# Optimization experiments

Measured on AMD Instinct MI355X. Metric: run time of the kernel, lower is better.

Reference implementation:

```python
import jax, jax.numpy as jnp
import numpy as np

EPS = 1e-5


def _bn_relu(y, g, beta, relu=True):
    # BatchNorm1d in training mode: biased batch stats over (B, V) per channel
    mean = jnp.mean(y, axis=(0, 2), keepdims=True)
    var = jnp.mean((y - mean) ** 2, axis=(0, 2), keepdims=True)
    out = (y - mean) * jax.lax.rsqrt(var + EPS) * g[None, :, None] + beta[None, :, None]
    return jnp.maximum(out, 0.0) if relu else out


def _spiral_conv(x, idx, w, b, g, beta):
    # x: (B,C,V), idx: (V,L) -> gather (B,C,V,L), row-major reshape to (B,C*L,V)
    B, C, V = x.shape
    L = idx.shape[1]
    neigh = x[:, :, idx].reshape(B, C * L, V)
    y = jnp.einsum('om,bmv->bov', w, neigh) + b[None, :, None]
    return _bn_relu(y, g, beta)


def _se(x, w1, w2):
    s = jnp.mean(x, axis=2)                              # (B,C)
    h = jnp.maximum(jnp.einsum('bc,rc->br', s, w1), 0.0)  # (B,r)
    s = jax.nn.sigmoid(jnp.einsum('br,cr->bc', h, w2))   # (B,C)
    return x * s[:, :, None]


def setup_inputs() -> dict:
    key = jax.random.key(0)
    ks = jax.random.split(key, 24)
    B, V, L, H = 2, 16384, 12, 256
    sc = 0.05
    inp = {
        'verts': jax.random.normal(ks[0], (B, V, 3), jnp.float32),
        'spirals': jax.random.randint(ks[1], (4, V, L), 0, V, jnp.int32),
        'enc0_w': jax.random.normal(ks[2], (H, 3 * L), jnp.float32) * sc,
        'enc0_b': jax.random.normal(ks[3], (H,), jnp.float32) * sc,
        'enc0_g': jnp.ones((H,), jnp.float32),
        'enc0_beta': jnp.zeros((H,), jnp.float32),
        'enc_w': jax.random.normal(ks[4], (3, H, H * L), jnp.float32) * sc,
        'enc_b': jax.random.normal(ks[5], (3, H), jnp.float32) * sc,
        'enc_g': jnp.ones((3, H), jnp.float32),
        'enc_beta': jnp.zeros((3, H), jnp.float32),
        'se_w1': jax.random.normal(ks[6], (4, H // 8, H), jnp.float32) * sc,
        'se_w2': jax.random.normal(ks[7], (4, H, H // 8), jnp.float32) * sc,
        'skip_w': jax.random.normal(ks[8], (3, H, 2 * H), jnp.float32) * sc,
        'skip_b': jax.random.normal(ks[9], (3, H), jnp.float32) * sc,
        'dec_w': jax.random.normal(ks[10], (3, H, H * L), jnp.float32) * sc,
        'dec_b': jax.random.normal(ks[11], (3, H), jnp.float32) * sc,
        'dec_g': jnp.ones((3, H), jnp.float32),
        'dec_beta': jnp.zeros((3, H), jnp.float32),
        'cls1_w': jax.random.normal(ks[12], (H // 2, H), jnp.float32) * sc,
        'cls1_b': jax.random.normal(ks[13], (H // 2,), jnp.float32) * sc,
        'cls1_g': jnp.ones((H // 2,), jnp.float32),
        'cls1_beta': jnp.zeros((H // 2,), jnp.float32),
        'cls2_w': jax.random.normal(ks[14], (H // 4, H // 2), jnp.float32) * sc,
        'cls2_b': jax.random.normal(ks[15], (H // 4,), jnp.float32) * sc,
        'cls2_g': jnp.ones((H // 4,), jnp.float32),
        'cls2_beta': jnp.zeros((H // 4,), jnp.float32),
        'cls3_w': jax.random.normal(ks[16], (1, H // 4), jnp.float32) * sc,
        'cls3_b': jax.random.normal(ks[17], (1,), jnp.float32) * sc,
    }
    return inp


def reference(verts, spirals, enc0_w, enc0_b, enc0_g, enc0_beta,
              enc_w, enc_b, enc_g, enc_beta, se_w1, se_w2,
              skip_w, skip_b, dec_w, dec_b, dec_g, dec_beta,
              cls1_w, cls1_b, cls1_g, cls1_beta,
              cls2_w, cls2_b, cls2_g, cls2_beta, cls3_w, cls3_b):
    x = jnp.transpose(verts, (0, 2, 1))  # (B,3,V)
    feats = []
    # encoder: 4 blocks, block0 has no residual (3 != 256)
    for i in range(4):
        if i == 0:
            out = _spiral_conv(x, spirals[0], enc0_w, enc0_b, enc0_g, enc0_beta)
        else:
            out = _spiral_conv(x, spirals[i], enc_w[i - 1], enc_b[i - 1], enc_g[i - 1], enc_beta[i - 1]) + x
        x = _se(out, se_w1[i], se_w2[i])
        feats.append(x)
    # decoder with skip-concat fusion, spirals[2],[1],[0] and feats[2],[1],[0]
    for i in range(3):
        feat = feats[2 - i]
        idx = spirals[2 - i]
        xc = jnp.concatenate([x, feat], axis=1)  # (B,512,V)
        x = jnp.einsum('oc,bcv->bov', skip_w[i], xc) + skip_b[i][None, :, None]
        x = _spiral_conv(x, idx, dec_w[i], dec_b[i], dec_g[i], dec_beta[i]) + x
    # classifier: 1x1 conv stack
    h = _bn_relu(jnp.einsum('oc,bcv->bov', cls1_w, x) + cls1_b[None, :, None], cls1_g, cls1_beta)
    h = _bn_relu(jnp.einsum('oc,bcv->bov', cls2_w, h) + cls2_b[None, :, None], cls2_g, cls2_beta)
    out = jnp.einsum('oc,bcv->bov', cls3_w, h) + cls3_b[None, :, None]  # (B,1,V)
    return out[:, 0, :]  # (B,V)
```

## Files before the change

### kernel.cpp

```cpp
#include <hip/hip_runtime.h>

typedef unsigned short u16;
using f16x8 = __attribute__((ext_vector_type(8))) _Float16;
using f32x4 = __attribute__((ext_vector_type(4))) float;

#define V_N 16384
#define M_N 32768

__device__ __forceinline__ float h2f(u16 u) {
  _Float16 h; __builtin_memcpy(&h, &u, 2); return (float)h;
}
__device__ __forceinline__ u16 f2h(float f) {
  _Float16 h = (_Float16)f; u16 u; __builtin_memcpy(&u, &h, 2); return u;
}

__device__ __forceinline__ void dma16(const u16* g, u16* l) {
  __builtin_amdgcn_global_load_lds(
      (const __attribute__((address_space(1))) void*)(const void*)g,
      (__attribute__((address_space(3))) void*)(void*)l, 16, 0, 0);
}

__global__ __launch_bounds__(256) void perm2_k(const float* __restrict__ w, u16* __restrict__ wp) {
  int o = blockIdx.x & 255, layer = blockIdx.x >> 8;
  int t = threadIdx.x;
  const float* src = w + ((size_t)layer * 256 + o) * 3072;
  u16* dst = wp + (size_t)layer * 786432;
  float2 v[6];
  #pragma unroll
  for (int q = 0; q < 6; ++q) v[q] = *(const float2*)(src + t * 12 + q * 2);
  const float* vf = (const float*)v;
  int lo = t & 31;
  #pragma unroll
  for (int m = 0; m < 12; ++m) {
    int kc = m * 8 + (t >> 5);
    dst[(size_t)kc * 8192 + o * 32 + lo] = f2h(vf[m]);
  }
}

__global__ __launch_bounds__(256) void permfr_k(const float* __restrict__ src, u16* __restrict__ dst,
                                                int O, int K) {
  int i = blockIdx.x * 256 + threadIdx.x;
  if (i >= (K << 8)) return;
  int j = i & 7, lq = (i >> 3) & 3, col = (i >> 5) & 255, kc = i >> 13;
  int k = kc * 32 + lq * 8 + j;
  float v = (col < O) ? src[(size_t)col * K + k] : 0.f;
  dst[i] = f2h(v);
}

__global__ __launch_bounds__(256) void wscale_k(const u16* __restrict__ w, const float* __restrict__ sig,
                                                const float* __restrict__ sigx,
                                                u16* __restrict__ o, int n, int sel) {
  int i = blockIdx.x * 256 + threadIdx.x;
  if (i >= n) return;
  float wv = h2f(w[i]);
  int k = (i >> 13) * 32 + ((i >> 3) & 3) * 8 + (i & 7);
  int c = k & 255;
  #pragma unroll
  for (int b = 0; b < 2; ++b) {
    float s;
    if (sel == 511 && k < 256) s = sigx ? sigx[b * 256 + c] : 1.f;
    else                       s = sig[b * 256 + c];
    o[(long)b * n + i] = f2h(wv * s);
  }
}

__global__ __launch_bounds__(256) void enc0_k(const float* __restrict__ verts, const int* __restrict__ sp,
                                              const float* __restrict__ w0, u16* __restrict__ y) {
  __shared__ float xs[32][36];
  int t = threadIdx.x;
  int r0 = blockIdx.x * 32;
  for (int s = t; s < 32 * 12; s += 256) {
    int row = s / 12, tt = s - row * 12;
    int gr = r0 + row;
    int b = gr >> 14, v = gr & (V_N - 1);
    int j = sp[tt * V_N + v];
    const float* p = verts + ((long)b * V_N + j) * 3;
    xs[row][tt]      = p[0];
    xs[row][12 + tt] = p[1];
    xs[row][24 + tt] = p[2];
  }
  __syncthreads();
  float w[36];
  #pragma unroll
  for (int k = 0; k < 36; ++k) w[k] = w0[t * 36 + k];
  for (int row = 0; row < 32; ++row) {
    float a = 0.f;
    #pragma unroll
    for (int k = 0; k < 36; ++k) a += w[k] * xs[row][k];
    y[(long)(r0 + row) * 256 + t] = f2h(a);
  }
}

template<int CT>
__global__ __launch_bounds__(512, 4) void gemm3_k(
    const u16* __restrict__ P0, const u16* __restrict__ P1, int lda,
    const int* __restrict__ sp, int L,
    const u16* __restrict__ Wt, long wstride,
    u16* __restrict__ Yb, const float* __restrict__ bias, int Ostore,
    float* __restrict__ stats)
{
  constexpr int KC   = CT >> 5;
  constexpr int PH   = (CT == 256) ? 4 : 2;
  constexpr int KCP  = KC / PH;
  constexpr int PROW = 64;
  __shared__ __align__(16) u16 lA[2][64 * PROW];
  const int tid  = threadIdx.x;
  const int wave = tid >> 6, lane = tid & 63;
  const int wn = wave * 32;
  const int lr = lane & 15, lq = lane >> 4;
  const int nwg = gridDim.x;
  const int wg = (blockIdx.x & 7) * (nwg >> 3) + (blockIdx.x >> 3);
  const int bm = wg * 64;
  const int batch = bm >> 14;
  const int vbase = bm & (V_N - 1);
  const int qrow = lane >> 3;
  const int qchunk = lane & 7;
  const bool gat = (sp != nullptr);
  const long rowb = (long)batch * V_N;
  const u16* Pd1 = P1 ? P1 : P0;
  const u16* Wb = Wt + (long)batch * wstride;
  const int NS = PH * L;

  const u16* bp[2];
  #pragma unroll
  for (int nt = 0; nt < 2; ++nt)
    bp[nt] = Wb + ((long)(wn + nt * 16 + lr) * 4 + lq) * 8;

  auto load_idx = [&](int tap) -> int {
    int v = 0;
    if (gat && lane < 8) v = sp[(long)tap * V_N + vbase + wave * 8 + lane];
    return v;
  };

  auto dma_st = [&](int sb, const u16* src, int idxreg, int ph) {
    u16* wb = lA[sb] + wave * (8 * PROW);
    int rloc = wave * 8 + qrow;
    long grow;
    if (gat) grow = rowb + (long)__shfl(idxreg, qrow, 64);
    else     grow = bm + rloc;
    const u16* gp = src + grow * lda + ph * PROW + ((qchunk ^ (rloc & 7)) << 3);
    dma16(gp, wb);
  };

  auto loadB = [&](int cb, f16x8 (&tB)[KCP * 2]) {
    #pragma unroll
    for (int kp = 0; kp < KCP; ++kp)
      #pragma unroll
      for (int nt = 0; nt < 2; ++nt)
        tB[kp * 2 + nt] = *(const f16x8*)(bp[nt] + (long)(cb + kp) * 8192);
  };

  f32x4 acc[4][2];
  #pragma unroll
  for (int i = 0; i < 4; ++i)
    #pragma unroll
    for (int j = 0; j < 2; ++j) acc[i][j] = (f32x4){0.f, 0.f, 0.f, 0.f};

  auto compute_st = [&](int sb, const f16x8 (&tB)[KCP * 2]) {
    #pragma unroll
    for (int kp = 0; kp < KCP; ++kp) {
      f16x8 a[4];
      #pragma unroll
      for (int mt = 0; mt < 4; ++mt) {
        int row = mt * 16 + lr;
        a[mt] = *(const f16x8*)(&lA[sb][row * PROW + (((kp * 4 + lq) ^ (row & 7)) << 3)]);
      }
      #pragma unroll
      for (int mt = 0; mt < 4; ++mt)
        #pragma unroll
        for (int nt = 0; nt < 2; ++nt)
          acc[mt][nt] = __builtin_amdgcn_mfma_f32_16x16x32_f16(a[mt], tB[kp * 2 + nt], acc[mt][nt], 0, 0, 0);
    }
  };

  f16x8 tBc[KCP * 2], tBn[KCP * 2];

  int idxC = load_idx(0);
  dma_st(0, P0, idxC, 0);
  loadB(0, tBc);
  int idxN = (gat && L > 1) ? load_idx(1) : idxC;

  int l = 0, ph = 0;
  for (int s = 0; s < NS; ++s) {
    int ln  = (l + 1 == L) ? 0 : l + 1;
    int phn = (l + 1 == L) ? ph + 1 : ph;
    __syncthreads();
    if (s + 1 < NS) {
      const u16* srcN = (!gat && ln > 0) ? Pd1 : P0;
      dma_st((s + 1) & 1, srcN, idxN, phn);
      loadB(ln * KC + phn * KCP, tBn);
    }
    int idxF = 0;
    if (gat && s + 2 < NS) {
      int l2 = (ln + 1 == L) ? 0 : ln + 1;
      idxF = load_idx(l2);
    }
    compute_st(s & 1, tBc);
    #pragma unroll
    for (int i = 0; i < KCP * 2; ++i) tBc[i] = tBn[i];
    idxN = idxF;
    l = ln; ph = phn;
  }

  #pragma unroll
  for (int nt = 0; nt < 2; ++nt) {
    int col = wn + nt * 16 + lr;
    if (col < Ostore) {
      float bv = bias ? bias[col] : 0.f;
      float s1 = 0.f, s2 = 0.f;
      #pragma unroll
      for (int mt = 0; mt < 4; ++mt) {
        #pragma unroll
        for (int rg = 0; rg < 4; ++rg) {
          int row = bm + mt * 16 + lq * 4 + rg;
          float v = acc[mt][nt][rg] + bv;
          Yb[(long)row * Ostore + col] = f2h(v);
          s1 += v; s2 += v * v;
        }
      }
      if (stats) {
        s1 += __shfl_xor(s1, 16); s1 += __shfl_xor(s1, 32);
        s2 += __shfl_xor(s2, 16); s2 += __shfl_xor(s2, 32);
        if (lq == 0) {
          atomicAdd(&stats[col], s1);
          atomicAdd(&stats[Ostore + col], s2);
        }
      }
    }
  }
}

__global__ __launch_bounds__(256) void stats2_k(const u16* __restrict__ y, float* __restrict__ st) {
  __shared__ float s1L[256], s2L[256];
  int tid = threadIdx.x;
  int ci = (tid & 63) * 4;
  int r0 = blockIdx.x * 64 + (tid >> 6);
  float a1[4] = {0,0,0,0}, a2[4] = {0,0,0,0};
  for (int it = 0; it < 16; ++it) {
    long i = ((long)r0 + it * 4) * 256 + ci;
    uint2 pv = *(const uint2*)(y + i);
    float v0 = h2f((u16)(pv.x & 0xffff)), v1 = h2f((u16)(pv.x >> 16));
    float v2 = h2f((u16)(pv.y & 0xffff)), v3 = h2f((u16)(pv.y >> 16));
    a1[0] += v0; a1[1] += v1; a1[2] += v2; a1[3] += v3;
    a2[0] += v0*v0; a2[1] += v1*v1; a2[2] += v2*v2; a2[3] += v3*v3;
  }
  s1L[tid] = 0.f; s2L[tid] = 0.f;
  __syncthreads();
  #pragma unroll
  for (int j = 0; j < 4; ++j) { atomicAdd(&s1L[ci + j], a1[j]); atomicAdd(&s2L[ci + j], a2[j]); }
  __syncthreads();
  atomicAdd(&st[tid], s1L[tid]);
  atomicAdd(&st[256 + tid], s2L[tid]);
}

__global__ __launch_bounds__(256) void bnrelu2_k(
    const u16* __restrict__ y, const float* __restrict__ st,
    const float* __restrict__ g, const float* __restrict__ be,
    const u16* __restrict__ resid, const float* __restrict__ rscale,
    u16* __restrict__ ob, float* __restrict__ ses, int O)
{
  __shared__ float sL[256];
  int tid = threadIdx.x;
  int tpr = O >> 2;
  int rpi = 256 / tpr;
  int ci = (tid & (tpr - 1)) * 4;
  int row0 = blockIdx.x * (rpi * 16);
  int r0 = row0 + (tid / tpr);
  int b = row0 >> 14;
  float mean[4], sc[4], sh[4], rs[4];
  #pragma unroll
  for (int j = 0; j < 4; ++j) {
    int c = ci + j;
    float m = st[c] * (1.f / 32768.f);
    float var = st[O + c] * (1.f / 32768.f) - m * m;
    mean[j] = m;
    sc[j] = rsqrtf(fmaxf(var, 0.f) + 1e-5f) * g[c];
    sh[j] = be[c];
    rs[j] = rscale ? rscale[b * 256 + c] : 1.f;
  }
  float ss[4] = {0,0,0,0};
  for (int it = 0; it < 16; ++it) {
    long i = ((long)r0 + (long)it * rpi) * O + ci;
    uint2 pv = *(const uint2*)(y + i);
    float v[4];
    v[0] = fmaxf((h2f((u16)(pv.x & 0xffff)) - mean[0]) * sc[0] + sh[0], 0.f);
    v[1] = fmaxf((h2f((u16)(pv.x >> 16))    - mean[1]) * sc[1] + sh[1], 0.f);
    v[2] = fmaxf((h2f((u16)(pv.y & 0xffff)) - mean[2]) * sc[2] + sh[2], 0.f);
    v[3] = fmaxf((h2f((u16)(pv.y >> 16))    - mean[3]) * sc[3] + sh[3], 0.f);
    if (resid) {
      uint2 rv = *(const uint2*)(resid + i);
      v[0] += h2f((u16)(rv.x & 0xffff)) * rs[0]; v[1] += h2f((u16)(rv.x >> 16)) * rs[1];
      v[2] += h2f((u16)(rv.y & 0xffff)) * rs[2]; v[3] += h2f((u16)(rv.y >> 16)) * rs[3];
    }
    uint2 pk;
    pk.x = (unsigned)f2h(v[0]) | ((unsigned)f2h(v[1]) << 16);
    pk.y = (unsigned)f2h(v[2]) | ((unsigned)f2h(v[3]) << 16);
    *(uint2*)(ob + i) = pk;
    #pragma unroll
    for (int j = 0; j < 4; ++j) ss[j] += v[j];
  }
  if (ses) {
    sL[tid] = 0.f;
    __syncthreads();
    #pragma unroll
    for (int j = 0; j < 4; ++j) atomicAdd(&sL[ci + j], ss[j]);
    __syncthreads();
    atomicAdd(&ses[b * O + tid], sL[tid]);
  }
}

__global__ void se_k(const float* __restrict__ ses, const float* __restrict__ w1,
                     const float* __restrict__ w2, float* __restrict__ sig)
{
  __shared__ float s[256];
  __shared__ float h[32];
  int b = blockIdx.x, t = threadIdx.x;
  s[t] = ses[b * 256 + t] * (1.f / 16384.f);
  __syncthreads();
  if (t < 32) {
    float a = 0.f;
    for (int c = 0; c < 256; ++c) a += w1[t * 256 + c] * s[c];
    h[t] = fmaxf(a, 0.f);
  }
  __syncthreads();
  float a = 0.f;
  #pragma unroll
  for (int r = 0; r < 32; ++r) a += w2[t * 32 + r] * h[r];
  sig[b * 256 + t] = 1.f / (1.f + expf(-a));
}

__global__ __launch_bounds__(256) void cls3_k(const u16* __restrict__ h2, const float* __restrict__ w,
                                              const float* __restrict__ b, float* __restrict__ out)
{
  __shared__ float ws[64];
  int t = threadIdx.x;
  if (t < 64) ws[t] = w[t];
  __syncthreads();
  int r = blockIdx.x * 256 + t;
  const u16* p = h2 + (long)r * 64;
  float a = b[0];
  #pragma unroll
  for (int c = 0; c < 64; ++c) a += ws[c] * h2f(p[c]);
  out[r] = a;
}

extern "C" void kernel_launch(void* const* d_in, const int* in_sizes, int n_in,
                              void* d_out, int out_size, void* d_ws, size_t ws_size,
                              hipStream_t stream)
{
  (void)in_sizes; (void)n_in; (void)out_size; (void)ws_size;
  const float* verts   = (const float*)d_in[0];
  const int*   spirals = (const int*)d_in[1];
  const float* enc0_w  = (const float*)d_in[2];
  const float* enc0_g  = (const float*)d_in[4];
  const float* enc0_be = (const float*)d_in[5];
  const float* enc_w   = (const float*)d_in[6];
  const float* enc_g   = (const float*)d_in[8];
  const float* enc_be  = (const float*)d_in[9];
  const float* se_w1   = (const float*)d_in[10];
  const float* se_w2   = (const float*)d_in[11];
  const float* skip_w  = (const float*)d_in[12];
  const float* skip_b  = (const float*)d_in[13];
  const float* dec_w   = (const float*)d_in[14];
  const float* dec_g   = (const float*)d_in[16];
  const float* dec_be  = (const float*)d_in[17];
  const float* cls1_w  = (const float*)d_in[18];
  const float* cls1_g  = (const float*)d_in[20];
  const float* cls1_be = (const float*)d_in[21];
  const float* cls2_w  = (const float*)d_in[22];
  const float* cls2_g  = (const float*)d_in[24];
  const float* cls2_be = (const float*)d_in[25];
  const float* cls3_w  = (const float*)d_in[26];
  const float* cls3_b  = (const float*)d_in[27];

  char* p = (char*)d_ws;
  auto alloc = [&](size_t n) { char* q = p; p += (n + 255) & ~(size_t)255; return q; };
  u16* wpe     = (u16*)alloc((size_t)6 * 256 * 3072 * 2);
  u16* wpe_s   = (u16*)alloc((size_t)3 * 2 * 256 * 3072 * 2);
  u16* skip_wb = (u16*)alloc((size_t)3 * 256 * 512 * 2);
  u16* skip_s  = (u16*)alloc((size_t)3 * 2 * 256 * 512 * 2);
  u16* cls1_wb = (u16*)alloc((size_t)256 * 256 * 2);
  u16* wp6     = (u16*)alloc((size_t)256 * 128 * 2);
  float* stats = (float*)alloc(2048);
  float* sesum = (float*)alloc(2048);
  float* sig   = (float*)alloc(4 * 2048);
  u16* out0 = (u16*)alloc((size_t)M_N * 256 * 2);
  u16* out1 = (u16*)alloc((size_t)M_N * 256 * 2);
  u16* out2 = (u16*)alloc((size_t)M_N * 256 * 2);
  u16* ct   = (u16*)alloc((size_t)M_N * 256 * 2);
  u16* tb   = (u16*)alloc((size_t)M_N * 256 * 2);
  u16* xd   = (u16*)alloc((size_t)M_N * 256 * 2);
  u16* outs[4] = {out0, out1, out2, ct};
  const size_t WENC = (size_t)256 * 3072;
  const size_t WSKP = (size_t)256 * 512;

  perm2_k<<<768, 256, 0, stream>>>(enc_w, wpe);
  perm2_k<<<768, 256, 0, stream>>>(dec_w, wpe + (size_t)3 * WENC);
  for (int s = 0; s < 3; ++s)
    permfr_k<<<512, 256, 0, stream>>>(skip_w + (size_t)s * 256 * 512,
                                      skip_wb + (size_t)s * WSKP, 256, 512);
  permfr_k<<<256, 256, 0, stream>>>(cls1_w, cls1_wb, 128, 256);
  permfr_k<<<128, 256, 0, stream>>>(cls2_w, wp6, 64, 128);

  hipMemsetAsync(stats, 0, 4096, stream);
  enc0_k<<<1024, 256, 0, stream>>>(verts, spirals, enc0_w, ct);
  stats2_k<<<512, 256, 0, stream>>>(ct, stats);
  bnrelu2_k<<<512, 256, 0, stream>>>(ct, stats, enc0_g, enc0_be, nullptr, nullptr, out0, sesum, 256);
  se_k<<<2, 256, 0, stream>>>(sesum, se_w1, se_w2, sig);

  for (int i = 1; i < 4; ++i) {
    wscale_k<<<3072, 256, 0, stream>>>(wpe + (size_t)(i - 1) * WENC, sig + (i - 1) * 512, nullptr,
                                       wpe_s + (size_t)(i - 1) * 2 * WENC, (int)WENC, 255);
    hipMemsetAsync(stats, 0, 4096, stream);
    gemm3_k<256><<<512, 512, 0, stream>>>(outs[i - 1], nullptr, 256,
                                          spirals + (size_t)i * V_N * 12, 12,
                                          wpe_s + (size_t)(i - 1) * 2 * WENC, (long)WENC,
                                          ct, nullptr, 256, stats);
    bnrelu2_k<<<512, 256, 0, stream>>>(ct, stats, enc_g + (i - 1) * 256, enc_be + (i - 1) * 256,
                                       outs[i - 1], sig + (i - 1) * 512, outs[i], sesum, 256);
    se_k<<<2, 256, 0, stream>>>(sesum, se_w1 + (size_t)i * 32 * 256,
                                se_w2 + (size_t)i * 256 * 32, sig + i * 512);
  }

  for (int i = 0; i < 3; ++i) {
    wscale_k<<<512, 256, 0, stream>>>(skip_wb + (size_t)i * WSKP, sig + (2 - i) * 512,
                                      (i == 0) ? (sig + 3 * 512) : nullptr,
                                      skip_s + (size_t)i * 2 * WSKP, (int)WSKP, 511);
    gemm3_k<256><<<512, 512, 0, stream>>>((i == 0) ? ct : xd, outs[2 - i], 256, nullptr, 2,
                                          skip_s + (size_t)i * 2 * WSKP, (long)WSKP,
                                          tb, skip_b + i * 256, 256, nullptr);
    hipMemsetAsync(stats, 0, 4096, stream);
    gemm3_k<256><<<512, 512, 0, stream>>>(tb, nullptr, 256,
                                          spirals + (size_t)(2 - i) * V_N * 12, 12,
                                          wpe + (size_t)(3 + i) * WENC, 0,
                                          outs[2 - i], nullptr, 256, stats);
    bnrelu2_k<<<512, 256, 0, stream>>>(outs[2 - i], stats, dec_g + i * 256, dec_be + i * 256,
                                       tb, nullptr, xd, nullptr, 256);
  }

  hipMemsetAsync(stats, 0, 4096, stream);
  gemm3_k<256><<<512, 512, 0, stream>>>(xd, nullptr, 256, nullptr, 1,
                                        cls1_wb, 0, ct, nullptr, 128, stats);
  bnrelu2_k<<<256, 256, 0, stream>>>(ct, stats, cls1_g, cls1_be, nullptr, nullptr, ct, nullptr, 128);
  hipMemsetAsync(stats, 0, 4096, stream);
  gemm3_k<128><<<512, 512, 0, stream>>>(ct, nullptr, 128, nullptr, 1,
                                        wp6, 0, tb, nullptr, 64, stats);
  bnrelu2_k<<<128, 256, 0, stream>>>(tb, stats, cls2_g, cls2_be, nullptr, nullptr, tb, nullptr, 64);
  cls3_k<<<128, 256, 0, stream>>>(tb, cls3_w, cls3_b, (float*)d_out);
}
```

Baseline: 914.3 us.

## Triple-buffer gathered A tiles in LDS with prefetch distance two

Replaces the double-buffered LDS pipeline in the spiral gather GEMM with a three-buffer ring. The gather DMA for stage s+2 is issued while stage s computes, and manual s_waitcnt/s_barrier with sched_barriers replace __syncthreads. The loop is unrolled by two so the B-register ping-pong works without copying tBn into tBc. The aim is to hide more of the irregular gather latency. In exchange it uses more LDS, which can lower occupancy, and the hard-coded vmcnt values depend on an exact per-thread count of outstanding loads, which is fragile across template instantiations.

```diff
diff --git a/kernel.cpp b/kernel.cpp
--- a/kernel.cpp
+++ b/kernel.cpp
@@ -103,7 +103,8 @@
   constexpr int PH   = (CT == 256) ? 4 : 2;
   constexpr int KCP  = KC / PH;
   constexpr int PROW = 64;
-  __shared__ __align__(16) u16 lA[2][64 * PROW];
+  constexpr int BUFE = 64 * PROW;
+  __shared__ __align__(16) u16 lA[3 * BUFE];
   const int tid  = threadIdx.x;
   const int wave = tid >> 6, lane = tid & 63;
   const int wn = wave * 32;
@@ -132,8 +133,8 @@
     return v;
   };
 
-  auto dma_st = [&](int sb, const u16* src, int idxreg, int ph) {
-    u16* wb = lA[sb] + wave * (8 * PROW);
+  auto dma_st = [&](u16* buf, const u16* src, int idxreg, int ph) {
+    u16* wb = buf + wave * (8 * PROW);
     int rloc = wave * 8 + qrow;
     long grow;
     if (gat) grow = rowb + (long)__shfl(idxreg, qrow, 64);
@@ -156,14 +157,14 @@
     #pragma unroll
     for (int j = 0; j < 2; ++j) acc[i][j] = (f32x4){0.f, 0.f, 0.f, 0.f};
 
-  auto compute_st = [&](int sb, const f16x8 (&tB)[KCP * 2]) {
+  auto compute_st = [&](const u16* buf, const f16x8 (&tB)[KCP * 2]) {
     #pragma unroll
     for (int kp = 0; kp < KCP; ++kp) {
       f16x8 a[4];
       #pragma unroll
       for (int mt = 0; mt < 4; ++mt) {
         int row = mt * 16 + lr;
-        a[mt] = *(const f16x8*)(&lA[sb][row * PROW + (((kp * 4 + lq) ^ (row & 7)) << 3)]);
+        a[mt] = *(const f16x8*)(&buf[row * PROW + (((kp * 4 + lq) ^ (row & 7)) << 3)]);
       }
       #pragma unroll
       for (int mt = 0; mt < 4; ++mt)
@@ -173,33 +174,51 @@
     }
   };
 
-  f16x8 tBc[KCP * 2], tBn[KCP * 2];
-
-  int idxC = load_idx(0);
-  dma_st(0, P0, idxC, 0);
-  loadB(0, tBc);
-  int idxN = (gat && L > 1) ? load_idx(1) : idxC;
-
-  int l = 0, ph = 0;
-  for (int s = 0; s < NS; ++s) {
-    int ln  = (l + 1 == L) ? 0 : l + 1;
-    int phn = (l + 1 == L) ? ph + 1 : ph;
-    __syncthreads();
-    if (s + 1 < NS) {
-      const u16* srcN = (!gat && ln > 0) ? Pd1 : P0;
-      dma_st((s + 1) & 1, srcN, idxN, phn);
-      loadB(ln * KC + phn * KCP, tBn);
+  f16x8 tA[KCP * 2], tB2[KCP * 2];
+
+  auto adv = [&](int& l, int& ph) { if (++l == L) { l = 0; ++ph; } };
+  int lB = 0, phB = 0; adv(lB, phB);
+  int lD = lB, phD = phB; adv(lD, phD);
+  int lI = lD; { int pT = phD; int lT = lI; adv(lT, pT); lI = lT; }
+  int idxN;
+
+  {
+    int i0 = load_idx(0);
+    int i1 = load_idx(lB);
+    idxN = load_idx(lD);
+    dma_st(lA, P0, i0, 0);
+    if (NS > 1) {
+      const u16* s1 = (!gat && lB > 0) ? Pd1 : P0;
+      dma_st(lA + BUFE, s1, i1, phB);
     }
-    int idxF = 0;
-    if (gat && s + 2 < NS) {
-      int l2 = (ln + 1 == L) ? 0 : ln + 1;
-      idxF = load_idx(l2);
+    __builtin_amdgcn_sched_barrier(0);
+    loadB(0, tA);
+    __builtin_amdgcn_sched_barrier(0);
+  }
+
+  auto stage = [&](int s, f16x8 (&tCur)[KCP * 2], f16x8 (&tNxt)[KCP * 2]) {
+    if (s + 1 < NS) asm volatile("s_waitcnt vmcnt(5)" ::: "memory");
+    else            asm volatile("s_waitcnt vmcnt(0)" ::: "memory");
+    asm volatile("s_waitcnt lgkmcnt(0)" ::: "memory");
+    __builtin_amdgcn_s_barrier();
+    __builtin_amdgcn_sched_barrier(0);
+    if (s + 1 < NS) loadB(lB * KC + phB * KCP, tNxt);
+    __builtin_amdgcn_sched_barrier(0);
+    int idxT = 0;
+    if (gat && s + 3 < NS) idxT = load_idx(lI);
+    if (s + 2 < NS) {
+      const u16* srcD = (!gat && lD > 0) ? Pd1 : P0;
+      dma_st(lA + ((s + 2) % 3) * BUFE, srcD, idxN, phD);
     }
-    compute_st(s & 1, tBc);
-    #pragma unroll
-    for (int i = 0; i < KCP * 2; ++i) tBc[i] = tBn[i];
-    idxN = idxF;
-    l = ln; ph = phn;
+    __builtin_amdgcn_sched_barrier(0);
+    compute_st(lA + (s % 3) * BUFE, tCur);
+    adv(lB, phB); adv(lD, phD); if (++lI == L) lI = 0;
+    idxN = idxT;
+  };
+
+  for (int s = 0; s < NS; s += 2) {
+    stage(s, tA, tB2);
+    stage(s + 1, tB2, tA);
   }
 
   #pragma unroll
```

Result: faster. 884.5 us (-3.3%).
